# Optimization experiments

Hardware: AMD Instinct MI355X
Metric: run time of the kernel (lower is better)

Reference implementation:

```python
import jax, jax.numpy as jnp
import numpy as np

HIDDEN = 32
DN = ('NCHW', 'OIHW', 'NCHW')


def setup_inputs() -> dict:
    key = jax.random.key(0)
    ks = jax.random.split(key, 16)
    B = 32768
    s = lambda *sh: 1.0 / np.sqrt(np.prod(sh[1:]) if len(sh) > 1 else sh[0])
    inp = {
        'x': jax.random.normal(ks[0], (B, 12, 3, 4, 4), jnp.float32),
        'hour': jax.random.uniform(ks[1], (B, 1), jnp.float32),
        # ConvLSTM cell: Conv2d(3+32 -> 4*32, k=3, pad=1)
        'conv_w': jax.random.normal(ks[2], (4 * HIDDEN, 3 + HIDDEN, 3, 3), jnp.float32) * 0.05,
        'conv_b': jnp.zeros((4 * HIDDEN,), jnp.float32),
        # hour embedding: Linear(1,16) -> ReLU -> Linear(16,32)
        'he_w1': jax.random.normal(ks[3], (1, 16), jnp.float32),
        'he_b1': jnp.zeros((16,), jnp.float32),
        'he_w2': jax.random.normal(ks[4], (16, 32), jnp.float32) * 0.25,
        'he_b2': jnp.zeros((32,), jnp.float32),
        # decoder: Linear(544,256) -> ReLU -> Linear(256,128) -> ReLU -> Linear(128,30) -> Sigmoid
        'd_w1': jax.random.normal(ks[5], (32 * 4 * 4 + 32, 256), jnp.float32) * 0.04,
        'd_b1': jnp.zeros((256,), jnp.float32),
        'd_w2': jax.random.normal(ks[6], (256, 128), jnp.float32) * 0.06,
        'd_b2': jnp.zeros((128,), jnp.float32),
        'd_w3': jax.random.normal(ks[7], (128, 30), jnp.float32) * 0.09,
        'd_b3': jnp.zeros((30,), jnp.float32),
    }
    return inp


def _convlstm_scan(x, conv_w, conv_b):
    B, T, C, H, W = x.shape
    h0 = jnp.zeros((B, HIDDEN, H, W), x.dtype)
    c0 = jnp.zeros((B, HIDDEN, H, W), x.dtype)

    def step(carry, xt):
        h, c = carry
        inp = jnp.concatenate([xt, h], axis=1)  # [B, 3+32, 4, 4]
        gates = jax.lax.conv_general_dilated(
            inp, conv_w, (1, 1), 'SAME', dimension_numbers=DN)
        gates = gates + conv_b[None, :, None, None]
        i, f, o, g = jnp.split(gates, 4, axis=1)
        c_next = jax.nn.sigmoid(f) * c + jax.nn.sigmoid(i) * jnp.tanh(g)
        h_next = jax.nn.sigmoid(o) * jnp.tanh(c_next)
        return (h_next, c_next), None

    xs = jnp.swapaxes(x, 0, 1)  # [T, B, C, H, W]
    (h, c), _ = jax.lax.scan(step, (h0, c0), xs)
    return h


def reference(x, hour, conv_w, conv_b, he_w1, he_b1, he_w2, he_b2,
              d_w1, d_b1, d_w2, d_b2, d_w3, d_b3):
    B = x.shape[0]
    h = _convlstm_scan(x, conv_w, conv_b)            # [B, 32, 4, 4]
    spatial = h.reshape(B, -1)                        # [B, 512]
    hf = jax.nn.relu(hour @ he_w1 + he_b1) @ he_w2 + he_b2  # [B, 32]
    z = jnp.concatenate([spatial, hf], axis=1)        # [B, 544]
    z = jax.nn.relu(z @ d_w1 + d_b1)
    z = jax.nn.relu(z @ d_w2 + d_b2)                  # (dropout is identity in eval)
    out = jax.nn.sigmoid(z @ d_w3 + d_b3)
    return out.reshape(B, 10, 3)
```

## Files before the change

### kernel.cpp

```cpp
#include <hip/hip_runtime.h>

typedef _Float16 f16;
typedef _Float16 f16x4 __attribute__((ext_vector_type(4)));
typedef _Float16 f16x8 __attribute__((ext_vector_type(8)));
typedef float f32x2 __attribute__((ext_vector_type(2)));
typedef float f32x4 __attribute__((ext_vector_type(4)));

#define MFMA16(a, b, c) __builtin_amdgcn_mfma_f32_16x16x32_f16((a), (b), (c), 0, 0, 0)

__device__ __forceinline__ float rcp_(float x) { return __builtin_amdgcn_rcpf(x); }
__device__ __forceinline__ float sigm(float v) { return rcp_(1.0f + __expf(-v)); }
__device__ __forceinline__ float tanh_(float v) { return 1.0f - 2.0f * rcp_(__expf(2.0f * v) + 1.0f); }
__device__ __forceinline__ float exp2_(float x) { return __builtin_amdgcn_exp2f(x); }

#define LOG2E 1.4426950408889634f
#define HCELL 80
#define HSAMP 2880
#define HBUFB 11520
#define XP0 23040
#define XBUFB 1152
#define AR 25344
#define WSO 25344
#define SMEMA 50688
#define NPAIR 4096
#define GRID_REC 768

extern "C" __global__ __launch_bounds__(256, 3)
void hwq_rec(const float* __restrict__ gx, const float* __restrict__ ghour,
             const float* __restrict__ gcw, const float* __restrict__ gcb,
             const float* __restrict__ ghw1, const float* __restrict__ ghb1,
             const float* __restrict__ ghw2, const float* __restrict__ ghb2,
             f16* __restrict__ wz)
{
  __shared__ __align__(16) char smem[SMEMA];
  const int tid = threadIdx.x;
  const int lane = tid & 63;
  const int wv = tid >> 6;
  const int lr = lane & 15;
  const int lk = lane >> 4;
  const int TOFF[9] = {0, 1, 2, 6, 7, 8, 12, 13, 14};
  const int pp0 = (lr >> 2) * 6 + (lr & 3);

  f16x8 Ax1[2], Ax2[2];
  {
    f16* axs = (f16*)(smem + WSO);
    for (int i = tid; i < 4096; i += 256) {
      int m = i >> 5, k = i & 31;
      int tau = k >> 2, sl = k & 3;
      int oc = ((m & 3) << 5) + (m >> 2);
      float sc = ((m & 3) == 3) ? (2.0f * LOG2E) : (-LOG2E);
      f16 v = (f16)0.0f;
      if (sl < 3) v = (f16)(sc * gcw[oc * 315 + sl * 9 + tau]);
      else if (tau == 4) v = (f16)(sc * gcb[oc]);
      axs[i] = v;
    }
    __syncthreads();
    #pragma unroll
    for (int mt = 0; mt < 2; ++mt) {
      Ax1[mt] = *(const f16x8*)(smem + WSO + (wv * 32 + mt * 16 + lr) * 64 + lk * 16);
      int m = wv * 32 + mt * 16 + lr;
      int oc = ((m & 3) << 5) + (m >> 2);
      float sc = ((m & 3) == 3) ? (2.0f * LOG2E) : (-LOG2E);
      f16x8 f = {(f16)0, (f16)0, (f16)0, (f16)0, (f16)0, (f16)0, (f16)0, (f16)0};
      if (lk == 0) {
        f[0] = (f16)(sc * gcw[oc * 315 + 8]);
        f[1] = (f16)(sc * gcw[oc * 315 + 17]);
        f[2] = (f16)(sc * gcw[oc * 315 + 26]);
      }
      Ax2[mt] = f;
    }
    __syncthreads();
  }
  f16x8 Ah[9][2];
  {
    f16* wst = (f16*)(smem + WSO);
    #pragma unroll
    for (int c = 0; c < 4; ++c) {
      for (int i = tid; i < 9216; i += 256) {
        int mrow = i / 288, rem = i - mrow * 288;
        int m = c * 32 + mrow;
        int oc = ((m & 3) << 5) + (m >> 2);
        float sc = ((m & 3) == 3) ? (2.0f * LOG2E) : (-LOG2E);
        wst[i] = (f16)(sc * gcw[oc * 315 + 27 + rem]);
      }
      __syncthreads();
      if (wv == c) {
        #pragma unroll
        for (int mt = 0; mt < 2; ++mt) {
          #pragma unroll
          for (int tap = 0; tap < 9; ++tap) {
            f16x8 f;
            #pragma unroll
            for (int j = 0; j < 8; ++j)
              f[j] = wst[(mt * 16 + lr) * 288 + (lk * 8 + j) * 9 + tap];
            Ah[tap][mt] = f;
          }
        }
      }
      __syncthreads();
    }
  }
  {
    float* za = (float*)smem;
    for (int i = tid; i < 12672; i += 256) za[i] = 0.0f;
    __syncthreads();
    {
      int ar = tid >> 7, xb = (tid >> 6) & 1, b = (tid >> 4) & 3, p = tid & 15;
      int cell = ((p >> 2) + 1) * 6 + (p & 3) + 1;
      *(f16*)(smem + ar * AR + XP0 + xb * XBUFB + b * 288 + cell * 8 + 6) = (f16)1.0f;
    }
    __syncthreads();
  }

  const int hb  = pp0 * HCELL + lk * 16;
  const int xpb = XP0 + pp0 * 8;
  const int wb  = (pp0 + 7) * HCELL + (wv * 8 + lk) * 2;
  const int xo0 = TOFF[2 * lk] * 8;
  const int xo1 = TOFF[2 * lk + 1] * 8;
  const bool stg = tid < 192;
  const int sb = tid / 48, srem = tid - sb * 48;
  const int sp = srem & 15, sic = srem >> 4;
  const int xdst = XP0 + sb * 288 + (((sp >> 2) + 1) * 6 + (sp & 3) + 1) * 8 + sic * 2;
  const int zb_ = tid >> 6, zc16 = (tid >> 2) & 15, zpart = tid & 3;
  const int zaddr = zb_ * HSAMP + ((zc16 >> 2) * 6 + (zc16 & 3) + 7) * HCELL + zpart * 16;

  const f32x4 Z0v = {0.f, 0.f, 0.f, 0.f};

#define XPH(ab, nt) { \
    const int base_ = (ab) + xrb + xpb + (nt) * 288; \
    f16x4 lo_ = *(const f16x4*)(smem + base_ + xo0); \
    f16x4 hi_ = *(const f16x4*)(smem + base_ + xo1); \
    f16x8 bf1_ = __builtin_shufflevector(lo_, hi_, 0, 1, 2, 3, 4, 5, 6, 7); \
    f16x4 l8_ = *(const f16x4*)(smem + base_ + 112); \
    f16x8 bf2_ = __builtin_shufflevector(l8_, l8_, 0, 1, 2, 3, 0, 1, 2, 3); \
    _Pragma("unroll") for (int mt = 0; mt < 2; ++mt) { \
      acc[mt][nt] = MFMA16(Ax1[mt], bf1_, Z0v); \
      acc[mt][nt] = MFMA16(Ax2[mt], bf2_, acc[mt][nt]); } }

#define TAPS(ab, nt) \
    _Pragma("unroll") for (int tap = 0; tap < 9; ++tap) { \
      f16x8 bf_ = *(const f16x8*)(smem + (ab) + rb + hb + (nt) * HSAMP + TOFF[tap] * HCELL); \
      _Pragma("unroll") for (int mt = 0; mt < 2; ++mt) \
        acc[mt][nt] = MFMA16(Ah[tap][mt], bf_, acc[mt][nt]); }

#define PRIO1 __builtin_amdgcn_s_setprio(1)
#define PRIO0 __builtin_amdgcn_s_setprio(0)

#define UPD_L(g, ab, mt, nt) { \
    float Ei = exp2_(acc[mt][nt][0]); \
    float Ef = exp2_(acc[mt][nt][1]); \
    float Eo = exp2_(acc[mt][nt][2]); \
    float Eg = exp2_(acc[mt][nt][3]); \
    float fg = rcp_(1.0f + Ef); \
    float pq = rcp_((1.0f + Ei) * (1.0f + Eg)); \
    float cn = fmaf(fg, cst[g][mt][nt], (2.0f * LOG2E) * ((Eg - 1.0f) * pq)); \
    cst[g][mt][nt] = cn; \
    float Ec = exp2_(cn); \
    *(f16*)(smem + (ab) + wbuf + wb + (nt) * HSAMP + (mt) * 8) = \
        (f16)((Ec - 1.0f) * rcp_((1.0f + Eo) * (1.0f + Ec))); }

#define UPD_G(g, bgv, mt, nt) { \
    float Ei = exp2_(acc[mt][nt][0]); \
    float Ef = exp2_(acc[mt][nt][1]); \
    float Eo = exp2_(acc[mt][nt][2]); \
    float Eg = exp2_(acc[mt][nt][3]); \
    float fg = rcp_(1.0f + Ef); \
    float pq = rcp_((1.0f + Ei) * (1.0f + Eg)); \
    float cn = fmaf(fg, cst[g][mt][nt], (2.0f * LOG2E) * ((Eg - 1.0f) * pq)); \
    float Ec = exp2_(cn); \
    wz[(size_t)((bgv) + (nt)) * 544 + (wv * 8 + (mt) * 4 + lk) * 16 + lr] = \
        (f16)((Ec - 1.0f) * rcp_((1.0f + Eo) * (1.0f + Ec))); }

  const int bid = blockIdx.x;
  const int q_ = NPAIR / GRID_REC;
  const int r_ = NPAIR - q_ * GRID_REC;
  const int myn = q_ + (bid < r_ ? 1 : 0);
  const int mys = (bid < r_) ? bid * (q_ + 1) : r_ * (q_ + 1) + (bid - r_) * q_;

  for (int pi = 0; pi < myn; ++pi) {
    const int pr = mys + pi;
    const int bgA = pr << 3;
    const int bgB = bgA + 4;
    const float* xsrcA = gx + (size_t)(bgA + sb) * 576 + srem;
    const float* xsrcB = gx + (size_t)(bgB + sb) * 576 + srem;

    {
      f32x2 z2 = {0.f, 0.f};
      *(f32x2*)(smem + zaddr) = z2;
      *(f32x2*)(smem + zaddr + 8) = z2;
      *(f32x2*)(smem + AR + zaddr) = z2;
      *(f32x2*)(smem + AR + zaddr + 8) = z2;
    }
    if (stg) {
      *(f16*)(smem + xdst) = (f16)xsrcA[0];
      *(f16*)(smem + AR + xdst) = (f16)xsrcB[0];
    }
    float cst[2][2][4];
    #pragma unroll
    for (int g = 0; g < 2; ++g)
      #pragma unroll
      for (int mt = 0; mt < 2; ++mt)
        #pragma unroll
        for (int nt = 0; nt < 4; ++nt) cst[g][mt][nt] = 0.0f;
    __syncthreads();

    for (int t = 0; t < 11; ++t) {
      const int rb   = (t & 1) * HBUFB;
      const int xrb  = (t & 1) * XBUFB;
      const int wbuf = HBUFB - rb;
      float xvA = 0.0f, xvB = 0.0f;
      if (stg) { xvA = xsrcA[(t + 1) * 48]; xvB = xsrcB[(t + 1) * 48]; }

      f32x4 acc[2][4];
      PRIO1;
      XPH(0, 0); TAPS(0, 0);
      XPH(0, 1); TAPS(0, 1);
      XPH(0, 2); TAPS(0, 2);
      XPH(0, 3); TAPS(0, 3);
      PRIO0;
      UPD_L(0, 0, 0, 0); UPD_L(0, 0, 1, 0);
      PRIO1; XPH(AR, 0); TAPS(AR, 0); PRIO0;
      UPD_L(0, 0, 0, 1); UPD_L(0, 0, 1, 1);
      PRIO1; XPH(AR, 1); TAPS(AR, 1); PRIO0;
      UPD_L(0, 0, 0, 2); UPD_L(0, 0, 1, 2);
      PRIO1; XPH(AR, 2); TAPS(AR, 2); PRIO0;
      UPD_L(0, 0, 0, 3); UPD_L(0, 0, 1, 3);
      PRIO1; XPH(AR, 3); TAPS(AR, 3); PRIO0;
      UPD_L(1, AR, 0, 0); UPD_L(1, AR, 1, 0);
      UPD_L(1, AR, 0, 1); UPD_L(1, AR, 1, 1);
      UPD_L(1, AR, 0, 2); UPD_L(1, AR, 1, 2);
      UPD_L(1, AR, 0, 3); UPD_L(1, AR, 1, 3);

      if (stg) {
        *(f16*)(smem + (XBUFB - xrb) + xdst) = (f16)xvA;
        *(f16*)(smem + AR + (XBUFB - xrb) + xdst) = (f16)xvB;
      }
      __syncthreads();
    }

    {
      const int rb  = HBUFB;
      const int xrb = XBUFB;
      f32x4 acc[2][4];
      PRIO1;
      XPH(0, 0); TAPS(0, 0);
      XPH(0, 1); TAPS(0, 1);
      XPH(0, 2); TAPS(0, 2);
      XPH(0, 3); TAPS(0, 3);
      PRIO0;
      UPD_G(0, bgA, 0, 0); UPD_G(0, bgA, 1, 0);
      PRIO1; XPH(AR, 0); TAPS(AR, 0); PRIO0;
      UPD_G(0, bgA, 0, 1); UPD_G(0, bgA, 1, 1);
      PRIO1; XPH(AR, 1); TAPS(AR, 1); PRIO0;
      UPD_G(0, bgA, 0, 2); UPD_G(0, bgA, 1, 2);
      PRIO1; XPH(AR, 2); TAPS(AR, 2); PRIO0;
      UPD_G(0, bgA, 0, 3); UPD_G(0, bgA, 1, 3);
      PRIO1; XPH(AR, 3); TAPS(AR, 3); PRIO0;
      UPD_G(1, bgB, 0, 0); UPD_G(1, bgB, 1, 0);
      UPD_G(1, bgB, 0, 1); UPD_G(1, bgB, 1, 1);
      UPD_G(1, bgB, 0, 2); UPD_G(1, bgB, 1, 2);
      UPD_G(1, bgB, 0, 3); UPD_G(1, bgB, 1, 3);

      {
        int b = tid >> 5, k2 = tid & 31;
        int smp = bgA + b;
        float h0 = ghour[smp];
        float a = ghb2[k2];
        #pragma unroll
        for (int ii = 0; ii < 16; ++ii) {
          float u = fmaxf(h0 * ghw1[ii] + ghb1[ii], 0.0f);
          a += u * ghw2[ii * 32 + k2];
        }
        wz[(size_t)smp * 544 + 512 + k2] = (f16)a;
      }
    }
  }
#undef XPH
#undef TAPS
#undef UPD_L
#undef UPD_G
#undef PRIO1
#undef PRIO0
}

extern "C" __global__ void hwq_prep(const float* __restrict__ gdw1,
                                    const float* __restrict__ gdw2,
                                    const float* __restrict__ gdw3,
                                    f16* __restrict__ w1t, f16* __restrict__ w2t,
                                    f16* __restrict__ w3t)
{
  int i0 = blockIdx.x * 256 + threadIdx.x;
  int stride = gridDim.x * 256;
  for (int idx = i0; idx < 139264; idx += stride) {
    int n = idx / 544, k = idx - n * 544;
    w1t[idx] = (f16)gdw1[k * 256 + n];
  }
  for (int idx = i0; idx < 32768; idx += stride) {
    int n = idx >> 8, k = idx & 255;
    w2t[idx] = (f16)gdw2[k * 128 + n];
  }
  for (int idx = i0; idx < 4096; idx += stride) {
    int n = idx >> 7, k = idx & 127;
    w3t[idx] = (n < 30) ? (f16)gdw3[k * 30 + n] : (f16)0.0f;
  }
}

extern "C" __global__ __launch_bounds__(256, 2)
void hwq_dec(const f16* __restrict__ wz, const f16* __restrict__ w1t,
             const f16* __restrict__ w2t, const f16* __restrict__ w3t,
             const float* __restrict__ gdb1, const float* __restrict__ gdb2,
             const float* __restrict__ gdb3, float* __restrict__ gout)
{
  __shared__ __align__(16) char smem[55296];
  f16* a1 = (f16*)smem;
  f16* a2 = (f16*)(smem + 35840);
  const int tid = threadIdx.x;
  const int lane = tid & 63;
  const int wv = tid >> 6;
  const int lr = lane & 15;
  const int lk = lane >> 4;
  const int s0 = blockIdx.x << 6;

  f32x4 acc1[4][4];
  #pragma unroll
  for (int nt = 0; nt < 4; ++nt) {
    float bb = gdb1[wv * 64 + nt * 16 + lr];
    f32x4 bv = {bb, bb, bb, bb};
    #pragma unroll
    for (int mt = 0; mt < 4; ++mt) acc1[mt][nt] = bv;
  }
  for (int kt = 0; kt < 17; ++kt) {
    f16x8 af[4];
    #pragma unroll
    for (int mt = 0; mt < 4; ++mt)
      af[mt] = *(const f16x8*)(wz + (size_t)(s0 + mt * 16 + lr) * 544 + kt * 32 + lk * 8);
    #pragma unroll
    for (int nt = 0; nt < 4; ++nt) {
      f16x8 bf = *(const f16x8*)(w1t + (size_t)(wv * 64 + nt * 16 + lr) * 544 + kt * 32 + lk * 8);
      #pragma unroll
      for (int mt = 0; mt < 4; ++mt)
        acc1[mt][nt] = MFMA16(af[mt], bf, acc1[mt][nt]);
    }
  }
  #pragma unroll
  for (int mt = 0; mt < 4; ++mt)
    #pragma unroll
    for (int nt = 0; nt < 4; ++nt) {
      int n = wv * 64 + nt * 16 + lr;
      #pragma unroll
      for (int r = 0; r < 4; ++r)
        a1[(mt * 16 + lk * 4 + r) * 280 + n] = (f16)fmaxf(acc1[mt][nt][r], 0.0f);
    }
  __syncthreads();

  f32x4 acc2[4][2];
  #pragma unroll
  for (int nt = 0; nt < 2; ++nt) {
    float bb = gdb2[wv * 32 + nt * 16 + lr];
    f32x4 bv = {bb, bb, bb, bb};
    #pragma unroll
    for (int mt = 0; mt < 4; ++mt) acc2[mt][nt] = bv;
  }
  for (int kt = 0; kt < 8; ++kt) {
    f16x8 af[4];
    #pragma unroll
    for (int mt = 0; mt < 4; ++mt)
      af[mt] = *(const f16x8*)(a1 + (mt * 16 + lr) * 280 + kt * 32 + lk * 8);
    #pragma unroll
    for (int nt = 0; nt < 2; ++nt) {
      f16x8 bf = *(const f16x8*)(w2t + (size_t)(wv * 32 + nt * 16 + lr) * 256 + kt * 32 + lk * 8);
      #pragma unroll
      for (int mt = 0; mt < 4; ++mt)
        acc2[mt][nt] = MFMA16(af[mt], bf, acc2[mt][nt]);
    }
  }
  __syncthreads();
  #pragma unroll
  for (int mt = 0; mt < 4; ++mt)
    #pragma unroll
    for (int nt = 0; nt < 2; ++nt) {
      int n = wv * 32 + nt * 16 + lr;
      #pragma unroll
      for (int r = 0; r < 4; ++r)
        a2[(mt * 16 + lk * 4 + r) * 152 + n] = (f16)fmaxf(acc2[mt][nt][r], 0.0f);
    }
  __syncthreads();

  if (wv < 2) {
    int n = wv * 16 + lr;
    float bb = (n < 30) ? gdb3[n] : 0.0f;
    f32x4 acc3[4];
    #pragma unroll
    for (int mt = 0; mt < 4; ++mt) { f32x4 bv = {bb, bb, bb, bb}; acc3[mt] = bv; }
    #pragma unroll
    for (int kt = 0; kt < 4; ++kt) {
      f16x8 bf = *(const f16x8*)(w3t + n * 128 + kt * 32 + lk * 8);
      #pragma unroll
      for (int mt = 0; mt < 4; ++mt) {
        f16x8 af = *(const f16x8*)(a2 + (mt * 16 + lr) * 152 + kt * 32 + lk * 8);
        acc3[mt] = MFMA16(af, bf, acc3[mt]);
      }
    }
    if (n < 30) {
      #pragma unroll
      for (int mt = 0; mt < 4; ++mt)
        #pragma unroll
        for (int r = 0; r < 4; ++r)
          gout[(size_t)(s0 + mt * 16 + lk * 4 + r) * 30 + n] = sigm(acc3[mt][r]);
    }
  }
}

typedef _Float16 f16x4m __attribute__((ext_vector_type(4)));
#define OFF_B 46080
#define SMEM_BYTES (46080 + 17408)

extern "C" __global__ __launch_bounds__(256, 1)
void hwq_fused_mono(const float* __restrict__ gx, const float* __restrict__ ghour,
               const float* __restrict__ gcw, const float* __restrict__ gcb,
               const float* __restrict__ ghw1, const float* __restrict__ ghb1,
               const float* __restrict__ ghw2, const float* __restrict__ ghb2,
               const float* __restrict__ gdw1, const float* __restrict__ gdb1,
               const float* __restrict__ gdw2, const float* __restrict__ gdb2,
               const float* __restrict__ gdw3, const float* __restrict__ gdb3,
               float* __restrict__ gout)
{
  __shared__ __align__(16) char smem[SMEM_BYTES];
  const int tid = threadIdx.x;
  const int lane = tid & 63;
  const int wv = tid >> 6;
  const int mg = wv & 1;
  const int ng = wv >> 1;
  const int lr = lane & 15;
  const int lk = lane >> 4;
  const int bg = blockIdx.x << 4;

  f16x8 Ah[9][4];
  {
    f16* wst = (f16*)(smem);
    #pragma unroll
    for (int c = 0; c < 2; ++c) {
      __syncthreads();
      for (int i = tid; i < 18432; i += 256) {
        int oc = i / 288, rem = i - oc * 288;
        wst[i] = (f16)gcw[(c * 64 + oc) * 315 + 27 + rem];
      }
      __syncthreads();
      #pragma unroll
      for (int g = 0; g < 2; ++g) {
        int ocl = g * 32 + mg * 16 + lr;
        #pragma unroll
        for (int tap = 0; tap < 9; ++tap) {
          f16x8 f;
          #pragma unroll
          for (int j = 0; j < 8; ++j)
            f[j] = wst[ocl * 288 + (lk * 8 + j) * 9 + tap];
          Ah[tap][c * 2 + g] = f;
        }
      }
    }
  }
  f16x8 Ax[4];
  {
    f16* xw = (f16*)(smem + OFF_B);
    __syncthreads();
    for (int i = tid; i < 3456; i += 256) {
      int oc = i / 27, rem = i - oc * 27;
      xw[i] = (f16)gcw[oc * 315 + rem];
    }
    __syncthreads();
    #pragma unroll
    for (int mt = 0; mt < 4; ++mt) {
      int oc = mt * 32 + mg * 16 + lr;
      f16x8 f;
      #pragma unroll
      for (int j = 0; j < 8; ++j) {
        int k = lk * 8 + j;
        int tap = (k * 11) >> 5;
        int ic = k - 3 * tap;
        f16 v = (f16)0.0f;
        if (k < 27) v = xw[oc * 27 + ic * 9 + tap];
        f[j] = v;
      }
      Ax[mt] = f;
    }
    __syncthreads();
  }

  float bias[4][4];
  #pragma unroll
  for (int mt = 0; mt < 4; ++mt)
    #pragma unroll
    for (int r = 0; r < 4; ++r)
      bias[mt][r] = gcb[mt * 32 + mg * 16 + lk * 4 + r];

  {
    float* za = (float*)smem;
    for (int i = tid; i < 11520; i += 256) za[i] = 0.0f;
    float* zb = (float*)(smem + OFF_B);
    for (int i = tid; i < 1152; i += 256) zb[i] = 0.0f;
    __syncthreads();
    for (int i = tid; i < 768; i += 256) {
      int b = i / 48, rem = i - b * 48;
      int pos = rem & 15;
      int ic = rem >> 4;
      int pp = (pos >> 2) * 6 + (pos & 3) + 7;
      *(f16*)(smem + OFF_B + b * 288 + pp * 8 + ic * 2) =
          (f16)gx[(size_t)(bg + b) * 576 + rem];
    }
    __syncthreads();
  }

  int hbase[8], xbase[8], wbase[8];
  #pragma unroll
  for (int nt = 0; nt < 8; ++nt) {
    int n = ng * 128 + nt * 16 + lr;
    int b = n >> 4, pos = n & 15;
    int pp0 = (pos >> 2) * 6 + (pos & 3);
    hbase[nt] = b * 2880 + pp0 * 80 + lk * 16;
    xbase[nt] = OFF_B + b * 288 + pp0 * 8;
    wbase[nt] = b * 2880 + (pp0 + 7) * 80 + (mg * 16 + lk * 4) * 2;
  }
  int xoff[8], xval[8];
  #pragma unroll
  for (int j = 0; j < 8; ++j) {
    int k = lk * 8 + j;
    int tap = (k * 11) >> 5;
    int ic = k - 3 * tap;
    xoff[j] = ((tap / 3) * 6 + (tap % 3)) * 8 + ic * 2;
    xval[j] = (k < 27);
  }

  const int TOFF[9] = {0, 1, 2, 6, 7, 8, 12, 13, 14};

  f32x4 cst[8];
  #pragma unroll
  for (int nt = 0; nt < 8; ++nt) { f32x4 z = {0.f, 0.f, 0.f, 0.f}; cst[nt] = z; }

  for (int t = 0; t < 12; ++t) {
    f32x4 acc[4][8];
    #pragma unroll
    for (int mt = 0; mt < 4; ++mt) {
      f32x4 bi = {bias[mt][0], bias[mt][1], bias[mt][2], bias[mt][3]};
      #pragma unroll
      for (int nt = 0; nt < 8; ++nt) acc[mt][nt] = bi;
    }
    #pragma unroll
    for (int tap = 0; tap < 9; ++tap) {
      #pragma unroll
      for (int nt = 0; nt < 8; ++nt) {
        f16x8 bf = *(const f16x8*)(smem + hbase[nt] + TOFF[tap] * 80);
        #pragma unroll
        for (int mt = 0; mt < 4; ++mt)
          acc[mt][nt] = MFMA16(Ah[tap][mt], bf, acc[mt][nt]);
      }
    }
    #pragma unroll
    for (int nt = 0; nt < 8; ++nt) {
      f16x8 bf;
      #pragma unroll
      for (int j = 0; j < 8; ++j) {
        int a = xval[j] ? (xbase[nt] + xoff[j]) : OFF_B;
        bf[j] = *(const f16*)(smem + a);
      }
      #pragma unroll
      for (int mt = 0; mt < 4; ++mt)
        acc[mt][nt] = MFMA16(Ax[mt], bf, acc[mt][nt]);
    }
    __syncthreads();

    #pragma unroll
    for (int nt = 0; nt < 8; ++nt) {
      f16 hh[4];
      #pragma unroll
      for (int r = 0; r < 4; ++r) {
        float ig = sigm(acc[0][nt][r]);
        float fg = sigm(acc[1][nt][r]);
        float og = sigm(acc[2][nt][r]);
        float gg = tanh_(acc[3][nt][r]);
        float cn = fg * cst[nt][r] + ig * gg;
        cst[nt][r] = cn;
        hh[r] = (f16)(og * tanh_(cn));
      }
      if (t < 11) {
        f16x4m hv = {hh[0], hh[1], hh[2], hh[3]};
        *(f16x4m*)(smem + wbase[nt]) = hv;
      } else {
        int n = ng * 128 + nt * 16 + lr;
        int b = n >> 4, pos = n & 15;
        int ch0 = mg * 16 + lk * 4;
        #pragma unroll
        for (int r = 0; r < 4; ++r)
          *(f16*)(smem + OFF_B + b * 1088 + (ch0 + r) * 32 + pos * 2) = hh[r];
      }
    }
    if (t < 11) {
      for (int i = tid; i < 768; i += 256) {
        int b = i / 48, rem = i - b * 48;
        int pos = rem & 15;
        int ic = rem >> 4;
        int pp = (pos >> 2) * 6 + (pos & 3) + 7;
        *(f16*)(smem + OFF_B + b * 288 + pp * 8 + ic * 2) =
            (f16)gx[(size_t)(bg + b) * 576 + (t + 1) * 48 + rem];
      }
    } else {
      for (int i = tid; i < 512; i += 256) {
        int b = i >> 5, k2 = i & 31;
        float h0 = ghour[bg + b];
        float a = ghb2[k2];
        #pragma unroll
        for (int ii = 0; ii < 16; ++ii) {
          float u = fmaxf(h0 * ghw1[ii] + ghb1[ii], 0.0f);
          a += u * ghw2[ii * 32 + k2];
        }
        *(f16*)(smem + OFF_B + b * 1088 + (512 + k2) * 2) = (f16)a;
      }
    }
    __syncthreads();
  }

  f16* zz  = (f16*)(smem + OFF_B);
  f16* wch = (f16*)(smem);
  f16* a1  = (f16*)(smem + 16384);
  f16* a2  = (f16*)(smem + 24576);
  f16* w3s = (f16*)(smem + 28672);

  f32x4 acc1[4];
  #pragma unroll
  for (int i = 0; i < 4; ++i) { f32x4 z = {0.f, 0.f, 0.f, 0.f}; acc1[i] = z; }
  for (int kt = 0; kt < 17; ++kt) {
    __syncthreads();
    for (int i = tid; i < 8192; i += 256) {
      int k = i >> 8, n = i & 255;
      wch[i] = (f16)gdw1[(kt * 32 + k) * 256 + n];
    }
    __syncthreads();
    f16x8 af = *(const f16x8*)((char*)zz + lr * 1088 + (kt * 32 + lk * 8) * 2);
    #pragma unroll
    for (int nt = 0; nt < 4; ++nt) {
      int n = (wv * 4 + nt) * 16 + lr;
      f16x8 bf;
      #pragma unroll
      for (int j = 0; j < 8; ++j) bf[j] = wch[(lk * 8 + j) * 256 + n];
      acc1[nt] = MFMA16(af, bf, acc1[nt]);
    }
  }
  __syncthreads();
  #pragma unroll
  for (int nt = 0; nt < 4; ++nt) {
    int n = (wv * 4 + nt) * 16 + lr;
    float bb = gdb1[n];
    #pragma unroll
    for (int r = 0; r < 4; ++r)
      a1[(lk * 4 + r) * 256 + n] = (f16)fmaxf(acc1[nt][r] + bb, 0.0f);
  }

  f32x4 acc2[2];
  #pragma unroll
  for (int i = 0; i < 2; ++i) { f32x4 z = {0.f, 0.f, 0.f, 0.f}; acc2[i] = z; }
  for (int kt = 0; kt < 8; ++kt) {
    __syncthreads();
    for (int i = tid; i < 4096; i += 256) {
      int k = i >> 7, n = i & 127;
      wch[i] = (f16)gdw2[(kt * 32 + k) * 128 + n];
    }
    __syncthreads();
    f16x8 af = *(const f16x8*)((char*)a1 + lr * 512 + (kt * 32 + lk * 8) * 2);
    #pragma unroll
    for (int nt = 0; nt < 2; ++nt) {
      int n = (wv * 2 + nt) * 16 + lr;
      f16x8 bf;
      #pragma unroll
      for (int j = 0; j < 8; ++j) bf[j] = wch[(lk * 8 + j) * 128 + n];
      acc2[nt] = MFMA16(af, bf, acc2[nt]);
    }
  }
  __syncthreads();
  #pragma unroll
  for (int nt = 0; nt < 2; ++nt) {
    int n = (wv * 2 + nt) * 16 + lr;
    float bb = gdb2[n];
    #pragma unroll
    for (int r = 0; r < 4; ++r)
      a2[(lk * 4 + r) * 128 + n] = (f16)fmaxf(acc2[nt][r] + bb, 0.0f);
  }
  __syncthreads();

  for (int i = tid; i < 4096; i += 256) {
    int k = i >> 5, n = i & 31;
    w3s[i] = (n < 30) ? (f16)gdw3[k * 30 + n] : (f16)0.0f;
  }
  __syncthreads();
  if (wv < 2) {
    f32x4 acc3 = {0.f, 0.f, 0.f, 0.f};
    int n = wv * 16 + lr;
    #pragma unroll
    for (int kt = 0; kt < 4; ++kt) {
      f16x8 af = *(const f16x8*)((char*)a2 + lr * 256 + (kt * 32 + lk * 8) * 2);
      f16x8 bf;
      #pragma unroll
      for (int j = 0; j < 8; ++j) bf[j] = w3s[(kt * 32 + lk * 8 + j) * 32 + n];
      acc3 = MFMA16(af, bf, acc3);
    }
    if (n < 30) {
      float bb = gdb3[n];
      #pragma unroll
      for (int r = 0; r < 4; ++r) {
        float v = sigm(acc3[r] + bb);
        gout[(size_t)(bg + lk * 4 + r) * 30 + n] = v;
      }
    }
  }
}

extern "C" void kernel_launch(void* const* d_in, const int* in_sizes, int n_in,
                              void* d_out, int out_size, void* d_ws, size_t ws_size,
                              hipStream_t stream) {
  (void)in_sizes; (void)n_in; (void)out_size;
  const size_t W1OFF = 35651584;
  const size_t W2OFF = W1OFF + 278528;
  const size_t W3OFF = W2OFF + 65536;
  const size_t NEED  = W3OFF + 8192;
  if (ws_size >= NEED) {
    f16* wzp = (f16*)d_ws;
    f16* w1t = (f16*)((char*)d_ws + W1OFF);
    f16* w2t = (f16*)((char*)d_ws + W2OFF);
    f16* w3t = (f16*)((char*)d_ws + W3OFF);
    hwq_prep<<<256, 256, 0, stream>>>((const float*)d_in[8], (const float*)d_in[10],
                                      (const float*)d_in[12], w1t, w2t, w3t);
    hwq_rec<<<GRID_REC, 256, 0, stream>>>(
        (const float*)d_in[0], (const float*)d_in[1], (const float*)d_in[2],
        (const float*)d_in[3], (const float*)d_in[4], (const float*)d_in[5],
        (const float*)d_in[6], (const float*)d_in[7], wzp);
    hwq_dec<<<512, 256, 0, stream>>>(wzp, w1t, w2t, w3t,
                                     (const float*)d_in[9], (const float*)d_in[11],
                                     (const float*)d_in[13], (float*)d_out);
  } else {
    hwq_fused_mono<<<2048, 256, 0, stream>>>(
        (const float*)d_in[0],  (const float*)d_in[1],  (const float*)d_in[2],
        (const float*)d_in[3],  (const float*)d_in[4],  (const float*)d_in[5],
        (const float*)d_in[6],  (const float*)d_in[7],  (const float*)d_in[8],
        (const float*)d_in[9],  (const float*)d_in[10], (const float*)d_in[11],
        (const float*)d_in[12], (const float*)d_in[13], (float*)d_out);
  }
}
```

Measured before the change: 633.0 us.

## Fold weight prep into recurrent kernel, peel first timestep, shrink decoder LDS

Removes the separate weight-transpose prep kernel and performs the decoder weight conversion inside the recurrent kernel's prologue, saving one launch. Peels timestep 0 of the ConvLSTM loop so that it runs only the input-projection MFMAs, skipping the hidden-state taps and the per-pair zeroing of the h buffer because h is zero at that step. Reduces the decoder's a2 row stride and shared memory size and raises its launch bounds to 3 blocks per CU to improve occupancy. The peeled step still reads the x-buffer layout, and skipping h zeroing relies on UPD_L overwriting every cell the taps read later.

```diff
diff --git a/kernel.cpp b/kernel.cpp
--- a/kernel.cpp
+++ b/kernel.cpp
@@ -30,7 +30,10 @@
              const float* __restrict__ gcw, const float* __restrict__ gcb,
              const float* __restrict__ ghw1, const float* __restrict__ ghb1,
              const float* __restrict__ ghw2, const float* __restrict__ ghb2,
-             f16* __restrict__ wz)
+             f16* __restrict__ wz,
+             const float* __restrict__ gdw1, const float* __restrict__ gdw2,
+             const float* __restrict__ gdw3,
+             f16* __restrict__ w1t, f16* __restrict__ w2t, f16* __restrict__ w3t)
 {
   __shared__ __align__(16) char smem[SMEMA];
   const int tid = threadIdx.x;
@@ -40,6 +43,23 @@
   const int lk = lane >> 4;
   const int TOFF[9] = {0, 1, 2, 6, 7, 8, 12, 13, 14};
   const int pp0 = (lr >> 2) * 6 + (lr & 3);
+
+  {
+    int i0 = blockIdx.x * 256 + tid;
+    const int stride = GRID_REC * 256;
+    for (int idx = i0; idx < 139264; idx += stride) {
+      int n = idx / 544, k = idx - n * 544;
+      w1t[idx] = (f16)gdw1[k * 256 + n];
+    }
+    for (int idx = i0; idx < 32768; idx += stride) {
+      int n = idx >> 8, k = idx & 255;
+      w2t[idx] = (f16)gdw2[k * 128 + n];
+    }
+    for (int idx = i0; idx < 4096; idx += stride) {
+      int n = idx >> 7, k = idx & 127;
+      w3t[idx] = (n < 30) ? (f16)gdw3[k * 30 + n] : (f16)0.0f;
+    }
+  }
 
   f16x8 Ax1[2], Ax2[2];
   {
@@ -121,8 +141,6 @@
   const int sb = tid / 48, srem = tid - sb * 48;
   const int sp = srem & 15, sic = srem >> 4;
   const int xdst = XP0 + sb * 288 + (((sp >> 2) + 1) * 6 + (sp & 3) + 1) * 8 + sic * 2;
-  const int zb_ = tid >> 6, zc16 = (tid >> 2) & 15, zpart = tid & 3;
-  const int zaddr = zb_ * HSAMP + ((zc16 >> 2) * 6 + (zc16 & 3) + 7) * HCELL + zpart * 16;
 
   const f32x4 Z0v = {0.f, 0.f, 0.f, 0.f};
 
@@ -184,13 +202,6 @@
     const float* xsrcA = gx + (size_t)(bgA + sb) * 576 + srem;
     const float* xsrcB = gx + (size_t)(bgB + sb) * 576 + srem;
 
-    {
-      f32x2 z2 = {0.f, 0.f};
-      *(f32x2*)(smem + zaddr) = z2;
-      *(f32x2*)(smem + zaddr + 8) = z2;
-      *(f32x2*)(smem + AR + zaddr) = z2;
-      *(f32x2*)(smem + AR + zaddr + 8) = z2;
-    }
     if (stg) {
       *(f16*)(smem + xdst) = (f16)xsrcA[0];
       *(f16*)(smem + AR + xdst) = (f16)xsrcB[0];
@@ -204,7 +215,34 @@
         for (int nt = 0; nt < 4; ++nt) cst[g][mt][nt] = 0.0f;
     __syncthreads();
 
-    for (int t = 0; t < 11; ++t) {
+    {
+      const int xrb  = 0;
+      const int wbuf = HBUFB;
+      float xvA = 0.0f, xvB = 0.0f;
+      if (stg) { xvA = xsrcA[48]; xvB = xsrcB[48]; }
+
+      f32x4 acc[2][4];
+      PRIO1;
+      XPH(0, 0); XPH(0, 1); XPH(0, 2); XPH(0, 3);
+      XPH(AR, 0); XPH(AR, 1); XPH(AR, 2); XPH(AR, 3);
+      PRIO0;
+      UPD_L(0, 0, 0, 0); UPD_L(0, 0, 1, 0);
+      UPD_L(0, 0, 0, 1); UPD_L(0, 0, 1, 1);
+      UPD_L(0, 0, 0, 2); UPD_L(0, 0, 1, 2);
+      UPD_L(0, 0, 0, 3); UPD_L(0, 0, 1, 3);
+      UPD_L(1, AR, 0, 0); UPD_L(1, AR, 1, 0);
+      UPD_L(1, AR, 0, 1); UPD_L(1, AR, 1, 1);
+      UPD_L(1, AR, 0, 2); UPD_L(1, AR, 1, 2);
+      UPD_L(1, AR, 0, 3); UPD_L(1, AR, 1, 3);
+
+      if (stg) {
+        *(f16*)(smem + XBUFB + xdst) = (f16)xvA;
+        *(f16*)(smem + AR + XBUFB + xdst) = (f16)xvB;
+      }
+      __syncthreads();
+    }
+
+    for (int t = 1; t < 11; ++t) {
       const int rb   = (t & 1) * HBUFB;
       const int xrb  = (t & 1) * XBUFB;
       const int wbuf = HBUFB - rb;
@@ -283,35 +321,13 @@
 #undef PRIO0
 }
 
-extern "C" __global__ void hwq_prep(const float* __restrict__ gdw1,
-                                    const float* __restrict__ gdw2,
-                                    const float* __restrict__ gdw3,
-                                    f16* __restrict__ w1t, f16* __restrict__ w2t,
-                                    f16* __restrict__ w3t)
-{
-  int i0 = blockIdx.x * 256 + threadIdx.x;
-  int stride = gridDim.x * 256;
-  for (int idx = i0; idx < 139264; idx += stride) {
-    int n = idx / 544, k = idx - n * 544;
-    w1t[idx] = (f16)gdw1[k * 256 + n];
-  }
-  for (int idx = i0; idx < 32768; idx += stride) {
-    int n = idx >> 8, k = idx & 255;
-    w2t[idx] = (f16)gdw2[k * 128 + n];
-  }
-  for (int idx = i0; idx < 4096; idx += stride) {
-    int n = idx >> 7, k = idx & 127;
-    w3t[idx] = (n < 30) ? (f16)gdw3[k * 30 + n] : (f16)0.0f;
-  }
-}
-
-extern "C" __global__ __launch_bounds__(256, 2)
+extern "C" __global__ __launch_bounds__(256, 3)
 void hwq_dec(const f16* __restrict__ wz, const f16* __restrict__ w1t,
              const f16* __restrict__ w2t, const f16* __restrict__ w3t,
              const float* __restrict__ gdb1, const float* __restrict__ gdb2,
              const float* __restrict__ gdb3, float* __restrict__ gout)
 {
-  __shared__ __align__(16) char smem[55296];
+  __shared__ __align__(16) char smem[53248];
   f16* a1 = (f16*)smem;
   f16* a2 = (f16*)(smem + 35840);
   const int tid = threadIdx.x;
@@ -382,7 +398,7 @@
       int n = wv * 32 + nt * 16 + lr;
       #pragma unroll
       for (int r = 0; r < 4; ++r)
-        a2[(mt * 16 + lk * 4 + r) * 152 + n] = (f16)fmaxf(acc2[mt][nt][r], 0.0f);
+        a2[(mt * 16 + lk * 4 + r) * 136 + n] = (f16)fmaxf(acc2[mt][nt][r], 0.0f);
     }
   __syncthreads();
 
@@ -397,7 +413,7 @@
       f16x8 bf = *(const f16x8*)(w3t + n * 128 + kt * 32 + lk * 8);
       #pragma unroll
       for (int mt = 0; mt < 4; ++mt) {
-        f16x8 af = *(const f16x8*)(a2 + (mt * 16 + lr) * 152 + kt * 32 + lk * 8);
+        f16x8 af = *(const f16x8*)(a2 + (mt * 16 + lr) * 136 + kt * 32 + lk * 8);
         acc3[mt] = MFMA16(af, bf, acc3[mt]);
       }
     }
@@ -726,12 +742,12 @@
     f16* w1t = (f16*)((char*)d_ws + W1OFF);
     f16* w2t = (f16*)((char*)d_ws + W2OFF);
     f16* w3t = (f16*)((char*)d_ws + W3OFF);
-    hwq_prep<<<256, 256, 0, stream>>>((const float*)d_in[8], (const float*)d_in[10],
-                                      (const float*)d_in[12], w1t, w2t, w3t);
     hwq_rec<<<GRID_REC, 256, 0, stream>>>(
         (const float*)d_in[0], (const float*)d_in[1], (const float*)d_in[2],
         (const float*)d_in[3], (const float*)d_in[4], (const float*)d_in[5],
-        (const float*)d_in[6], (const float*)d_in[7], wzp);
+        (const float*)d_in[6], (const float*)d_in[7], wzp,
+        (const float*)d_in[8], (const float*)d_in[10], (const float*)d_in[12],
+        w1t, w2t, w3t);
     hwq_dec<<<512, 256, 0, stream>>>(wzp, w1t, w2t, w3t,
                                      (const float*)d_in[9], (const float*)d_in[11],
                                      (const float*)d_in[13], (float*)d_out);
```

Result: faster. 607.2 us (-4.1%).
